# Optimization experiments

Hardware: AMD Instinct MI355X
Metric: run time of the kernel (lower is better)

Reference implementation:

```python
import jax, jax.numpy as jnp
import numpy as np

B, C, H, W = 4, 256, 48, 48
HEADS, DIM_HEAD, SCALE = 8, 64, 10.0
INNER = HEADS * DIM_HEAD
EPS = 1e-12


def setup_inputs() -> dict:
    key = jax.random.key(0)
    k1, k2, k3, k4 = jax.random.split(key, 4)
    x = jax.random.normal(k1, (B, C, H, W), dtype=jnp.float32)
    # 1x1 conv weights stored as [out_ch, in_ch]
    w_qkv = jax.random.normal(k2, (3 * INNER, C), dtype=jnp.float32) * (1.0 / np.sqrt(C))
    w_out = jax.random.normal(k3, (C, INNER), dtype=jnp.float32) * (1.0 / np.sqrt(INNER))
    b_out = jax.random.normal(k4, (C,), dtype=jnp.float32) * 0.01
    return {"x": x, "w_qkv": w_qkv, "w_out": w_out, "b_out": b_out}


def _l2norm(t):
    # normalize along last axis, clamping the norm at EPS (matches torch l2norm)
    denom = jnp.maximum(jnp.linalg.norm(t, axis=-1, keepdims=True), EPS)
    return t / denom


def reference(x, w_qkv, w_out, b_out):
    b, c, h, w = x.shape
    n = h * w
    # 1x1 conv QKV projection: [B, 3*INNER, H, W]
    qkv = jnp.einsum('oc,bchw->bohw', w_qkv, x)
    q, k, v = jnp.split(qkv, 3, axis=1)
    # [B, heads, dim_head, N] -> [B, heads, N, dim_head]
    def to_bhnd(t):
        return t.reshape(b, HEADS, DIM_HEAD, n).transpose(0, 1, 3, 2)
    q = _l2norm(to_bhnd(q))
    k = _l2norm(to_bhnd(k))
    v = to_bhnd(v)
    sim = jnp.einsum('bhid,bhjd->bhij', q, k) * SCALE  # [B,h,N,N]
    attn = jax.nn.softmax(sim, axis=-1)
    out = jnp.einsum('bhij,bhjd->bhid', attn, v)  # [B,h,N,d]
    # back to [B, INNER, H, W]
    out = out.transpose(0, 1, 3, 2).reshape(b, INNER, h, w)
    # 1x1 conv output projection with bias
    out = jnp.einsum('oc,bchw->bohw', w_out, out) + b_out[None, :, None, None]
    return out
```

## Files before the change

kernel.cpp:

```cpp
#include <hip/hip_runtime.h>

typedef unsigned short u16;
typedef __attribute__((ext_vector_type(8))) short bf16x8;
typedef __attribute__((ext_vector_type(4))) float f32x4;

#define MFMA16(A,B,C) __builtin_amdgcn_mfma_f32_16x16x32_bf16(A,B,C,0,0,0)

#define B_ 4
#define C_ 256
#define N_ 2304
#define HEADS_ 8
#define DH_ 64
#define INNER_ 512
#define SCALE_LOG2E 14.426950408889634f

__device__ __forceinline__ u16 f2bf(float f) {
    union { float f; unsigned int u; } v; v.f = f;
    unsigned int r = v.u + 0x7fffu + ((v.u >> 16) & 1u);
    return (u16)(r >> 16);
}
__device__ __forceinline__ unsigned int pk2(float a, float b) {
    union { float f; unsigned int u; } va, vb; va.f = a; vb.f = b;
    return __builtin_amdgcn_perm(vb.u + 0x8000u, va.u + 0x8000u, 0x07060302u);
}

__global__ __launch_bounds__(256) void k_prep(const float* __restrict__ x,
                                              u16* __restrict__ xT,
                                              const float* __restrict__ w_qkv,
                                              u16* __restrict__ wqb,
                                              const float* __restrict__ w_out,
                                              u16* __restrict__ wob) {
    __shared__ float tile[64][65];
    int idx = blockIdx.x;
    int t = threadIdx.x;
    if (idx < 576) {
        int b = idx / 144, rem = idx % 144;
        int n0 = (rem >> 2) * 64, c0 = (rem & 3) * 64;
        const float* xb = x + (size_t)b * C_ * N_;
        u16* xTb = xT + (size_t)b * N_ * C_;
        int r = t >> 4;
        int q4 = (t & 15) * 4;
#pragma unroll
        for (int pass = 0; pass < 4; ++pass) {
            int c = r + pass * 16;
            float4 v = *(const float4*)(xb + (size_t)(c0 + c) * N_ + n0 + q4);
            tile[c][q4+0] = v.x; tile[c][q4+1] = v.y; tile[c][q4+2] = v.z; tile[c][q4+3] = v.w;
        }
        __syncthreads();
#pragma unroll
        for (int pass = 0; pass < 4; ++pass) {
            int n = r + pass * 16;
            ushort4 o;
            o.x = f2bf(tile[q4+0][n]); o.y = f2bf(tile[q4+1][n]);
            o.z = f2bf(tile[q4+2][n]); o.w = f2bf(tile[q4+3][n]);
            *(ushort4*)(xTb + (size_t)(n0 + n) * C_ + c0 + q4) = o;
        }
    } else if (idx < 960) {
        int i = (idx - 576) * 256 + t;
        float4 v = ((const float4*)w_qkv)[i];
        ushort4 o;
        o.x = f2bf(v.x); o.y = f2bf(v.y); o.z = f2bf(v.z); o.w = f2bf(v.w);
        ((ushort4*)wqb)[i] = o;
    } else {
        int i = (idx - 960) * 256 + t;
        float4 v = ((const float4*)w_out)[i];
        ushort4 o;
        o.x = f2bf(v.x); o.y = f2bf(v.y); o.z = f2bf(v.z); o.w = f2bf(v.w);
        ((ushort4*)wob)[i] = o;
    }
}

__global__ __launch_bounds__(256) void k_qkv(const u16* __restrict__ w_qkv,
                                             const u16* __restrict__ xT,
                                             u16* __restrict__ Qn,
                                             u16* __restrict__ Kn,
                                             u16* __restrict__ Vt) {
    __shared__ __align__(16) u16 Wt[64][264];
    __shared__ __align__(16) u16 Xt[64][264];
    int mt = blockIdx.x, nt = blockIdx.y, b = blockIdx.z;
    int tid = threadIdx.x;
    int wv = tid >> 6, lane = tid & 63;
    int col = lane & 15, quad = lane >> 4;
    int o0 = mt * 64;
    const u16* wtile = w_qkv + (size_t)o0 * C_;
    const u16* xtile = xT + ((size_t)b * N_ + nt*64) * C_;
#pragma unroll
    for (int p = 0; p < 8; ++p) {
        int c = p * 256 + tid;
        int row = c >> 5, seg = c & 31;
        *(uint4*)(&Wt[row][seg*8]) = *(const uint4*)(wtile + (size_t)row * C_ + seg*8);
        *(uint4*)(&Xt[row][seg*8]) = *(const uint4*)(xtile + (size_t)row * C_ + seg*8);
    }
    __syncthreads();
    f32x4 z = {0.f, 0.f, 0.f, 0.f};
    f32x4 acc[4]; acc[0]=z; acc[1]=z; acc[2]=z; acc[3]=z;
#pragma unroll
    for (int ks = 0; ks < 8; ++ks) {
        bf16x8 bfrag = *(const bf16x8*)(&Xt[wv*16 + col][ks*32 + quad*8]);
#pragma unroll
        for (int mb = 0; mb < 4; ++mb) {
            bf16x8 afrag = *(const bf16x8*)(&Wt[mb*16 + col][ks*32 + quad*8]);
            acc[mb] = MFMA16(afrag, bfrag, acc[mb]);
        }
    }
    int n = nt * 64 + wv * 16 + col;
    int which = mt >> 3, h = mt & 7;
    if (which < 2) {
        float s = 0.f;
#pragma unroll
        for (int mb = 0; mb < 4; ++mb)
#pragma unroll
            for (int r = 0; r < 4; ++r) s += acc[mb][r] * acc[mb][r];
        s += __shfl_xor(s, 16);
        s += __shfl_xor(s, 32);
        float inv = 1.f / fmaxf(sqrtf(s), 1e-12f);
        u16* dst = (which == 0 ? Qn : Kn) + (((size_t)b * HEADS_ + h) * N_ + n) * DH_;
#pragma unroll
        for (int mb = 0; mb < 4; ++mb) {
            ushort4 o;
            o.x = f2bf(acc[mb][0] * inv); o.y = f2bf(acc[mb][1] * inv);
            o.z = f2bf(acc[mb][2] * inv); o.w = f2bf(acc[mb][3] * inv);
            *(ushort4*)(dst + mb*16 + quad*4) = o;
        }
    } else {
        u16* dst = Vt + ((size_t)b * HEADS_ + h) * (size_t)DH_ * N_;
#pragma unroll
        for (int mb = 0; mb < 4; ++mb)
#pragma unroll
            for (int r = 0; r < 4; ++r)
                dst[(size_t)(mb*16 + quad*4 + r) * N_ + n] = f2bf(acc[mb][r]);
    }
}

__global__ __launch_bounds__(256) void k_attn(const u16* __restrict__ Qn,
                                              const u16* __restrict__ Kn,
                                              const u16* __restrict__ Vt,
                                              u16* __restrict__ AO) {
    __shared__ __align__(16) u16 Kt[64][72];
    __shared__ __align__(16) u16 Vtl[64][72];
    __shared__ __align__(16) u16 plds[4][16][72];
    int head_lin = blockIdx.x & 31;
    int qt = blockIdx.x >> 5;
    int b = head_lin >> 3, h = head_lin & 7;
    int tid = threadIdx.x;
    int wv = tid >> 6, lane = tid & 63;
    int col = lane & 15, quad = lane >> 4;
    size_t head = (size_t)b * HEADS_ + h;
    const u16* Qh = Qn + head * (size_t)N_ * DH_;
    const u16* Kh = Kn + head * (size_t)N_ * DH_;
    const u16* Vh = Vt + head * (size_t)DH_ * N_;
    int q0 = qt * 64 + wv * 16;
    bf16x8 qf0 = *(const bf16x8*)(Qh + (size_t)(q0 + col) * DH_ + quad*8);
    bf16x8 qf1 = *(const bf16x8*)(Qh + (size_t)(q0 + col) * DH_ + 32 + quad*8);
    f32x4 z = {0.f, 0.f, 0.f, 0.f};
    f32x4 O[4]; O[0]=z; O[1]=z; O[2]=z; O[3]=z;
    float l_i = 0.f;
    int vrow0 = tid >> 3, vseg = tid & 7;
    int krow0 = tid >> 3, kseg = tid & 7;
    const u16* ksrc0 = Kh + (size_t)tid * 8;
    const u16* vsrc0 = Vh + (size_t)vrow0 * N_ + vseg * 8;

    uint4 kreg0 = *(const uint4*)(ksrc0);
    uint4 kreg1 = *(const uint4*)(ksrc0 + 2048);
    uint4 vreg0 = *(const uint4*)(vsrc0);
    uint4 vreg1 = *(const uint4*)(vsrc0 + (size_t)32 * N_);

    for (int kt = 0; kt < N_/64; ++kt) {
        *(uint4*)(&Kt[krow0][kseg*8])      = kreg0;
        *(uint4*)(&Kt[32 + krow0][kseg*8]) = kreg1;
        *(uint4*)(&Vtl[vrow0][vseg*8])      = vreg0;
        *(uint4*)(&Vtl[32 + vrow0][vseg*8]) = vreg1;
        __syncthreads();
        int ktn = kt + 1 < N_/64 ? kt + 1 : kt;
        kreg0 = *(const uint4*)(ksrc0 + (size_t)ktn * 4096);
        kreg1 = *(const uint4*)(ksrc0 + (size_t)ktn * 4096 + 2048);
        vreg0 = *(const uint4*)(vsrc0 + ktn * 64);
        vreg1 = *(const uint4*)(vsrc0 + (size_t)32 * N_ + ktn * 64);
        float rs = 0.f;
#pragma unroll
        for (int nb = 0; nb < 4; ++nb) {
            f32x4 a = z;
            a = MFMA16(*(const bf16x8*)(&Kt[nb*16 + col][quad*8]), qf0, a);
            a = MFMA16(*(const bf16x8*)(&Kt[nb*16 + col][32 + quad*8]), qf1, a);
            float p0 = exp2f(fmaf(a[0], SCALE_LOG2E, -SCALE_LOG2E));
            float p1 = exp2f(fmaf(a[1], SCALE_LOG2E, -SCALE_LOG2E));
            float p2 = exp2f(fmaf(a[2], SCALE_LOG2E, -SCALE_LOG2E));
            float p3 = exp2f(fmaf(a[3], SCALE_LOG2E, -SCALE_LOG2E));
            rs += (p0 + p1) + (p2 + p3);
            uint2 w;
            w.x = pk2(p0, p1);
            w.y = pk2(p2, p3);
            *(uint2*)(&plds[wv][col][nb*16 + quad*4]) = w;
        }
        l_i += rs;
        __asm__ volatile("" ::: "memory");
#pragma unroll
        for (int ks = 0; ks < 2; ++ks) {
            bf16x8 pf = *(const bf16x8*)(&plds[wv][col][ks*32 + quad*8]);
#pragma unroll
            for (int nb = 0; nb < 4; ++nb) {
                bf16x8 vf = *(const bf16x8*)(&Vtl[nb*16 + col][ks*32 + quad*8]);
                O[nb] = MFMA16(vf, pf, O[nb]);
            }
        }
        __asm__ volatile("" ::: "memory");
        __syncthreads();
    }
    l_i += __shfl_xor(l_i, 16);
    l_i += __shfl_xor(l_i, 32);
    float linv = 1.f / l_i;
    u16* dst = AO + ((size_t)b * N_ + q0 + col) * INNER_ + h * DH_;
#pragma unroll
    for (int nb = 0; nb < 4; ++nb) {
        uint2 w;
        w.x = pk2(O[nb][0] * linv, O[nb][1] * linv);
        w.y = pk2(O[nb][2] * linv, O[nb][3] * linv);
        *(uint2*)(dst + nb*16 + quad*4) = w;
    }
}

__global__ __launch_bounds__(256) void k_proj(const u16* __restrict__ w_out,
                                              const float* __restrict__ b_out,
                                              const u16* __restrict__ AO,
                                              float* __restrict__ out) {
    __shared__ __align__(16) u16 Wt[64][264];
    __shared__ __align__(16) u16 At[64][264];
    int mt = blockIdx.x, nt = blockIdx.y, b = blockIdx.z;
    int tid = threadIdx.x;
    int wv = tid >> 6, lane = tid & 63;
    int col = lane & 15, quad = lane >> 4;
    int o0b = mt * 64;
    const u16* wtile = w_out + (size_t)o0b * INNER_;
    const u16* atile = AO + ((size_t)b * N_ + nt*64) * INNER_;
    f32x4 z = {0.f, 0.f, 0.f, 0.f};
    f32x4 acc[4]; acc[0]=z; acc[1]=z; acc[2]=z; acc[3]=z;
#pragma unroll
    for (int half = 0; half < 2; ++half) {
        if (half) __syncthreads();
#pragma unroll
        for (int p = 0; p < 8; ++p) {
            int c = p * 256 + tid;
            int row = c >> 5, seg = c & 31;
            *(uint4*)(&Wt[row][seg*8]) =
                *(const uint4*)(wtile + (size_t)row * INNER_ + half*256 + seg*8);
            *(uint4*)(&At[row][seg*8]) =
                *(const uint4*)(atile + (size_t)row * INNER_ + half*256 + seg*8);
        }
        __syncthreads();
#pragma unroll
        for (int ks = 0; ks < 8; ++ks) {
            bf16x8 af = *(const bf16x8*)(&Wt[wv*16 + col][ks*32 + quad*8]);
#pragma unroll
            for (int nb = 0; nb < 4; ++nb) {
                bf16x8 bfv = *(const bf16x8*)(&At[nb*16 + col][ks*32 + quad*8]);
                acc[nb] = MFMA16(af, bfv, acc[nb]);
            }
        }
    }
    int o0 = o0b + wv * 16;
    float bias[4];
#pragma unroll
    for (int r = 0; r < 4; ++r) bias[r] = b_out[o0 + quad*4 + r];
    float* dst = out + ((size_t)b * C_ + o0) * N_ + nt*64;
#pragma unroll
    for (int nb = 0; nb < 4; ++nb)
#pragma unroll
        for (int r = 0; r < 4; ++r)
            dst[(size_t)(quad*4 + r) * N_ + nb*16 + col] = acc[nb][r] + bias[r];
}

extern "C" void kernel_launch(void* const* d_in, const int* in_sizes, int n_in,
                              void* d_out, int out_size, void* d_ws, size_t ws_size,
                              hipStream_t stream) {
    const float* x     = (const float*)d_in[0];
    const float* w_qkv = (const float*)d_in[1];
    const float* w_out = (const float*)d_in[2];
    const float* b_out = (const float*)d_in[3];
    float* out = (float*)d_out;

    char* ws = (char*)d_ws;
    u16* xT  = (u16*)(ws);
    u16* Qn  = (u16*)(ws + 4718592);
    u16* Kn  = (u16*)(ws + 14155776);
    u16* Vt  = (u16*)(ws + 23592960);
    u16* AO  = (u16*)(ws + 33030144);
    u16* wqb = (u16*)(ws + 42467328);
    u16* wob = (u16*)(ws + 43253760);

    hipLaunchKernelGGL(k_prep, dim3(1088), dim3(256), 0, stream, x, xT, w_qkv, wqb, w_out, wob);
    hipLaunchKernelGGL(k_qkv,  dim3(24, N_/64, B_), dim3(256), 0, stream, wqb, xT, Qn, Kn, Vt);
    hipLaunchKernelGGL(k_attn, dim3((N_/64) * 32), dim3(256), 0, stream, Qn, Kn, Vt, AO);
    hipLaunchKernelGGL(k_proj, dim3(C_/64, N_/64, B_), dim3(256), 0, stream, wob, b_out, AO, out);
}
```

Before: 197.3 us.

## Process two query sub-tiles per wave in attention to reuse K/V fragments

The attention kernel now uses 128-thread blocks in which each of two waves handles 32 query rows as two 16-row sub-tiles. Each K and V fragment read from LDS feeds two MFMAs instead of one, which halves LDS read traffic per unit of math. Each thread now stages four K and four V vectors per tile instead of two each. The costs are higher register pressure and fewer waves per block to hide latency, with the same grid size.

After: 218.7 us. +10.9%, slower.

```diff
diff --git a/kernel.cpp b/kernel.cpp
--- a/kernel.cpp
+++ b/kernel.cpp
@@ -132,13 +132,13 @@
     }
 }
 
-__global__ __launch_bounds__(256) void k_attn(const u16* __restrict__ Qn,
+__global__ __launch_bounds__(128) void k_attn(const u16* __restrict__ Qn,
                                               const u16* __restrict__ Kn,
                                               const u16* __restrict__ Vt,
                                               u16* __restrict__ AO) {
     __shared__ __align__(16) u16 Kt[64][72];
     __shared__ __align__(16) u16 Vtl[64][72];
-    __shared__ __align__(16) u16 plds[4][16][72];
+    __shared__ __align__(16) u16 plds[2][32][72];
     int head_lin = blockIdx.x & 31;
     int qt = blockIdx.x >> 5;
     int b = head_lin >> 3, h = head_lin & 7;
@@ -149,73 +149,103 @@
     const u16* Qh = Qn + head * (size_t)N_ * DH_;
     const u16* Kh = Kn + head * (size_t)N_ * DH_;
     const u16* Vh = Vt + head * (size_t)DH_ * N_;
-    int q0 = qt * 64 + wv * 16;
-    bf16x8 qf0 = *(const bf16x8*)(Qh + (size_t)(q0 + col) * DH_ + quad*8);
-    bf16x8 qf1 = *(const bf16x8*)(Qh + (size_t)(q0 + col) * DH_ + 32 + quad*8);
+    int q0 = qt * 64 + wv * 32;
+    bf16x8 qfA0 = *(const bf16x8*)(Qh + (size_t)(q0 + col) * DH_ + quad*8);
+    bf16x8 qfA1 = *(const bf16x8*)(Qh + (size_t)(q0 + col) * DH_ + 32 + quad*8);
+    bf16x8 qfB0 = *(const bf16x8*)(Qh + (size_t)(q0 + 16 + col) * DH_ + quad*8);
+    bf16x8 qfB1 = *(const bf16x8*)(Qh + (size_t)(q0 + 16 + col) * DH_ + 32 + quad*8);
     f32x4 z = {0.f, 0.f, 0.f, 0.f};
-    f32x4 O[4]; O[0]=z; O[1]=z; O[2]=z; O[3]=z;
-    float l_i = 0.f;
-    int vrow0 = tid >> 3, vseg = tid & 7;
-    int krow0 = tid >> 3, kseg = tid & 7;
+    f32x4 OA[4], OB[4];
+#pragma unroll
+    for (int i = 0; i < 4; ++i) { OA[i] = z; OB[i] = z; }
+    float lA = 0.f, lB = 0.f;
+    int srow = tid >> 3, sseg = tid & 7;
     const u16* ksrc0 = Kh + (size_t)tid * 8;
-    const u16* vsrc0 = Vh + (size_t)vrow0 * N_ + vseg * 8;
-
-    uint4 kreg0 = *(const uint4*)(ksrc0);
-    uint4 kreg1 = *(const uint4*)(ksrc0 + 2048);
-    uint4 vreg0 = *(const uint4*)(vsrc0);
-    uint4 vreg1 = *(const uint4*)(vsrc0 + (size_t)32 * N_);
+    const u16* vsrc0 = Vh + (size_t)srow * N_ + sseg * 8;
+
+    uint4 k0 = *(const uint4*)(ksrc0);
+    uint4 k1 = *(const uint4*)(ksrc0 + 1024);
+    uint4 k2 = *(const uint4*)(ksrc0 + 2048);
+    uint4 k3 = *(const uint4*)(ksrc0 + 3072);
+    uint4 v0 = *(const uint4*)(vsrc0);
+    uint4 v1 = *(const uint4*)(vsrc0 + (size_t)16 * N_);
+    uint4 v2 = *(const uint4*)(vsrc0 + (size_t)32 * N_);
+    uint4 v3 = *(const uint4*)(vsrc0 + (size_t)48 * N_);
 
     for (int kt = 0; kt < N_/64; ++kt) {
-        *(uint4*)(&Kt[krow0][kseg*8])      = kreg0;
-        *(uint4*)(&Kt[32 + krow0][kseg*8]) = kreg1;
-        *(uint4*)(&Vtl[vrow0][vseg*8])      = vreg0;
-        *(uint4*)(&Vtl[32 + vrow0][vseg*8]) = vreg1;
+        *(uint4*)(&Kt[srow][sseg*8])      = k0;
+        *(uint4*)(&Kt[16 + srow][sseg*8]) = k1;
+        *(uint4*)(&Kt[32 + srow][sseg*8]) = k2;
+        *(uint4*)(&Kt[48 + srow][sseg*8]) = k3;
+        *(uint4*)(&Vtl[srow][sseg*8])      = v0;
+        *(uint4*)(&Vtl[16 + srow][sseg*8]) = v1;
+        *(uint4*)(&Vtl[32 + srow][sseg*8]) = v2;
+        *(uint4*)(&Vtl[48 + srow][sseg*8]) = v3;
         __syncthreads();
         int ktn = kt + 1 < N_/64 ? kt + 1 : kt;
-        kreg0 = *(const uint4*)(ksrc0 + (size_t)ktn * 4096);
-        kreg1 = *(const uint4*)(ksrc0 + (size_t)ktn * 4096 + 2048);
-        vreg0 = *(const uint4*)(vsrc0 + ktn * 64);
-        vreg1 = *(const uint4*)(vsrc0 + (size_t)32 * N_ + ktn * 64);
-        float rs = 0.f;
+        k0 = *(const uint4*)(ksrc0 + (size_t)ktn * 4096);
+        k1 = *(const uint4*)(ksrc0 + (size_t)ktn * 4096 + 1024);
+        k2 = *(const uint4*)(ksrc0 + (size_t)ktn * 4096 + 2048);
+        k3 = *(const uint4*)(ksrc0 + (size_t)ktn * 4096 + 3072);
+        v0 = *(const uint4*)(vsrc0 + ktn * 64);
+        v1 = *(const uint4*)(vsrc0 + (size_t)16 * N_ + ktn * 64);
+        v2 = *(const uint4*)(vsrc0 + (size_t)32 * N_ + ktn * 64);
+        v3 = *(const uint4*)(vsrc0 + (size_t)48 * N_ + ktn * 64);
+        float rsA = 0.f, rsB = 0.f;
 #pragma unroll
         for (int nb = 0; nb < 4; ++nb) {
-            f32x4 a = z;
-            a = MFMA16(*(const bf16x8*)(&Kt[nb*16 + col][quad*8]), qf0, a);
-            a = MFMA16(*(const bf16x8*)(&Kt[nb*16 + col][32 + quad*8]), qf1, a);
-            float p0 = exp2f(fmaf(a[0], SCALE_LOG2E, -SCALE_LOG2E));
-            float p1 = exp2f(fmaf(a[1], SCALE_LOG2E, -SCALE_LOG2E));
-            float p2 = exp2f(fmaf(a[2], SCALE_LOG2E, -SCALE_LOG2E));
-            float p3 = exp2f(fmaf(a[3], SCALE_LOG2E, -SCALE_LOG2E));
-            rs += (p0 + p1) + (p2 + p3);
-            uint2 w;
-            w.x = pk2(p0, p1);
-            w.y = pk2(p2, p3);
-            *(uint2*)(&plds[wv][col][nb*16 + quad*4]) = w;
-        }
-        l_i += rs;
+            bf16x8 kf0 = *(const bf16x8*)(&Kt[nb*16 + col][quad*8]);
+            bf16x8 kf1 = *(const bf16x8*)(&Kt[nb*16 + col][32 + quad*8]);
+            f32x4 a = MFMA16(kf0, qfA0, z);
+            a = MFMA16(kf1, qfA1, a);
+            f32x4 c = MFMA16(kf0, qfB0, z);
+            c = MFMA16(kf1, qfB1, c);
+            float a0 = exp2f(fmaf(a[0], SCALE_LOG2E, -SCALE_LOG2E));
+            float a1 = exp2f(fmaf(a[1], SCALE_LOG2E, -SCALE_LOG2E));
+            float a2 = exp2f(fmaf(a[2], SCALE_LOG2E, -SCALE_LOG2E));
+            float a3 = exp2f(fmaf(a[3], SCALE_LOG2E, -SCALE_LOG2E));
+            float c0 = exp2f(fmaf(c[0], SCALE_LOG2E, -SCALE_LOG2E));
+            float c1 = exp2f(fmaf(c[1], SCALE_LOG2E, -SCALE_LOG2E));
+            float c2 = exp2f(fmaf(c[2], SCALE_LOG2E, -SCALE_LOG2E));
+            float c3 = exp2f(fmaf(c[3], SCALE_LOG2E, -SCALE_LOG2E));
+            rsA += (a0 + a1) + (a2 + a3);
+            rsB += (c0 + c1) + (c2 + c3);
+            uint2 wA, wB;
+            wA.x = pk2(a0, a1); wA.y = pk2(a2, a3);
+            wB.x = pk2(c0, c1); wB.y = pk2(c2, c3);
+            *(uint2*)(&plds[wv][col][nb*16 + quad*4]) = wA;
+            *(uint2*)(&plds[wv][16 + col][nb*16 + quad*4]) = wB;
+        }
+        lA += rsA; lB += rsB;
         __asm__ volatile("" ::: "memory");
 #pragma unroll
         for (int ks = 0; ks < 2; ++ks) {
-            bf16x8 pf = *(const bf16x8*)(&plds[wv][col][ks*32 + quad*8]);
+            bf16x8 pfA = *(const bf16x8*)(&plds[wv][col][ks*32 + quad*8]);
+            bf16x8 pfB = *(const bf16x8*)(&plds[wv][16 + col][ks*32 + quad*8]);
 #pragma unroll
             for (int nb = 0; nb < 4; ++nb) {
                 bf16x8 vf = *(const bf16x8*)(&Vtl[nb*16 + col][ks*32 + quad*8]);
-                O[nb] = MFMA16(vf, pf, O[nb]);
+                OA[nb] = MFMA16(vf, pfA, OA[nb]);
+                OB[nb] = MFMA16(vf, pfB, OB[nb]);
             }
         }
         __asm__ volatile("" ::: "memory");
         __syncthreads();
     }
-    l_i += __shfl_xor(l_i, 16);
-    l_i += __shfl_xor(l_i, 32);
-    float linv = 1.f / l_i;
-    u16* dst = AO + ((size_t)b * N_ + q0 + col) * INNER_ + h * DH_;
+    lA += __shfl_xor(lA, 16); lA += __shfl_xor(lA, 32);
+    lB += __shfl_xor(lB, 16); lB += __shfl_xor(lB, 32);
+    float linvA = 1.f / lA, linvB = 1.f / lB;
+    u16* dstA = AO + ((size_t)b * N_ + q0 + col) * INNER_ + h * DH_;
+    u16* dstB = AO + ((size_t)b * N_ + q0 + 16 + col) * INNER_ + h * DH_;
 #pragma unroll
     for (int nb = 0; nb < 4; ++nb) {
-        uint2 w;
-        w.x = pk2(O[nb][0] * linv, O[nb][1] * linv);
-        w.y = pk2(O[nb][2] * linv, O[nb][3] * linv);
-        *(uint2*)(dst + nb*16 + quad*4) = w;
+        uint2 wA, wB;
+        wA.x = pk2(OA[nb][0] * linvA, OA[nb][1] * linvA);
+        wA.y = pk2(OA[nb][2] * linvA, OA[nb][3] * linvA);
+        wB.x = pk2(OB[nb][0] * linvB, OB[nb][1] * linvB);
+        wB.y = pk2(OB[nb][2] * linvB, OB[nb][3] * linvB);
+        *(uint2*)(dstA + nb*16 + quad*4) = wA;
+        *(uint2*)(dstB + nb*16 + quad*4) = wB;
     }
 }
 
@@ -289,6 +319,6 @@
 
     hipLaunchKernelGGL(k_prep, dim3(1088), dim3(256), 0, stream, x, xT, w_qkv, wqb, w_out, wob);
     hipLaunchKernelGGL(k_qkv,  dim3(24, N_/64, B_), dim3(256), 0, stream, wqb, xT, Qn, Kn, Vt);
-    hipLaunchKernelGGL(k_attn, dim3((N_/64) * 32), dim3(256), 0, stream, Qn, Kn, Vt, AO);
+    hipLaunchKernelGGL(k_attn, dim3((N_/64) * 32), dim3(128), 0, stream, Qn, Kn, Vt, AO);
     hipLaunchKernelGGL(k_proj, dim3(C_/64, N_/64, B_), dim3(256), 0, stream, wob, b_out, AO, out);
 }
```
